# Kernel tuning notes

Measured on AMD Instinct MI355X. Metric: run time of the kernel, lower is better.

The kernel has to match this reference:

```python
import jax, jax.numpy as jnp
import numpy as np

N, E = 50000, 800000
DN, DE, H, C = 64, 64, 4, 2
DH = DN // H


def setup_inputs() -> dict:
    key = jax.random.key(0)
    ks = jax.random.split(key, 12)
    def lin(k, fan_in, fan_out):
        return jax.random.normal(k, (fan_in, fan_out), dtype=jnp.float32) / np.sqrt(fan_in)
    return {
        "node_features": jax.random.normal(ks[0], (N, DN), dtype=jnp.float32),
        "edge_features": jax.random.normal(ks[1], (E, DE), dtype=jnp.float32),
        "edge_index": jax.random.randint(ks[2], (2, E), 0, N, dtype=jnp.int64),
        "Wq": lin(ks[3], DN, DN),
        "Wk": lin(ks[4], DN, DN),
        "Wv": lin(ks[5], DN, DN),
        "We": lin(ks[6], DE, DN),
        "Wo": lin(ks[7], DN, DN),
        "W1": lin(ks[8], 2 * DN + DE, DE),
        "b1": jnp.zeros((DE,), dtype=jnp.float32),
        "W2": lin(ks[9], DE, C),
        "b2": jnp.zeros((C,), dtype=jnp.float32),
    }


def reference(node_features, edge_features, edge_index, Wq, Wk, Wv, We, Wo, W1, b1, W2, b2):
    n = node_features.shape[0]
    src, tgt = edge_index[0], edge_index[1]

    # --- NodeAttention: multi-head attention over incoming edges ---
    q = (node_features @ Wq).reshape(n, H, DH)
    k = (node_features @ Wk).reshape(n, H, DH)
    v = (node_features @ Wv).reshape(n, H, DH)
    ep = (edge_features @ We).reshape(-1, H, DH)          # [E,H,DH]

    scores = jnp.sum(q[tgt] * (k[src] + ep), axis=-1) / np.sqrt(DH)  # [E,H]
    smax = jax.ops.segment_max(scores, tgt, num_segments=n)          # [N,H]
    ex = jnp.exp(scores - smax[tgt])
    denom = jax.ops.segment_sum(ex, tgt, num_segments=n)
    alpha = ex / (denom[tgt] + 1e-9)                                 # [E,H]

    msg = (alpha[..., None] * (v[src] + ep)).reshape(-1, H * DH)     # [E,DN]
    agg = jax.ops.segment_sum(msg, tgt, num_segments=n)              # [N,DN]
    new_nodes = node_features + agg @ Wo                             # residual

    # --- edge classifier: gather endpoints, concat edge feats, MLP+GELU ---
    edge_repr = jnp.concatenate([new_nodes[src], new_nodes[tgt], edge_features], axis=-1)
    h = jax.nn.gelu(edge_repr @ W1 + b1, approximate=False)
    return h @ W2 + b2
```

## Files before the change

kernel.cpp:

```cpp
#include <hip/hip_runtime.h>
#include <math.h>

typedef __attribute__((ext_vector_type(8))) short bf16x8;
typedef __attribute__((ext_vector_type(4))) float f32x4;

__device__ __forceinline__ short f2bf(float f) {
    unsigned u = __float_as_uint(f);
    unsigned r = (u + 0x7FFFu + ((u >> 16) & 1u)) >> 16;
    return (short)r;
}
__device__ __forceinline__ float bf2f(short s) {
    return __uint_as_float(((unsigned)(unsigned short)s) << 16);
}

__device__ __forceinline__ int swz(int row, int kbyte) {
    return kbyte ^ ((row & 7) << 4);
}

__global__ __launch_bounds__(256) void hist_kernel(
    const int* __restrict__ eidx, int* __restrict__ cnt, int E)
{
    for (long e = (long)blockIdx.x * blockDim.x + threadIdx.x; e < E;
         e += (long)gridDim.x * blockDim.x)
        atomicAdd(&cnt[eidx[E + e]], 1);
}

__global__ __launch_bounds__(256) void scanA_kernel(
    const int* __restrict__ cnt, int* __restrict__ tmp, int* __restrict__ bsum, int N)
{
    __shared__ int sa[256], sb_[256];
    int t = threadIdx.x;
    int i = blockIdx.x * 256 + t;
    int val = (i < N) ? cnt[i] : 0;
    sa[t] = val;
    __syncthreads();
    int* src = sa; int* dst = sb_;
    for (int off = 1; off < 256; off <<= 1) {
        int v2 = src[t];
        if (t >= off) v2 += src[t - off];
        dst[t] = v2;
        __syncthreads();
        int* tm = src; src = dst; dst = tm;
    }
    if (i < N) tmp[i] = src[t];
    if (t == 255) bsum[blockIdx.x] = src[255];
}

__global__ __launch_bounds__(256) void scanB_kernel(
    const int* __restrict__ bsum, int* __restrict__ boff, int NB)
{
    __shared__ int sa[256], sb_[256];
    int t = threadIdx.x;
    int val = (t < NB) ? bsum[t] : 0;
    sa[t] = val;
    __syncthreads();
    int* src = sa; int* dst = sb_;
    for (int off = 1; off < 256; off <<= 1) {
        int v2 = src[t];
        if (t >= off) v2 += src[t - off];
        dst[t] = v2;
        __syncthreads();
        int* tm = src; src = dst; dst = tm;
    }
    if (t < NB) boff[t] = src[t] - val;
}

__global__ __launch_bounds__(256) void scanC_kernel(
    const int* __restrict__ cnt, const int* __restrict__ tmp,
    const int* __restrict__ boff, int* __restrict__ cursor, int N)
{
    int i = blockIdx.x * 256 + threadIdx.x;
    if (i < N) cursor[i] = tmp[i] - cnt[i] + boff[blockIdx.x];
}

__global__ __launch_bounds__(256) void scatter_kernel(
    const int* __restrict__ eidx, int* __restrict__ cursor,
    int4* __restrict__ sortedq, int E)
{
    for (long e = (long)blockIdx.x * blockDim.x + threadIdx.x; e < E;
         e += (long)gridDim.x * blockDim.x) {
        int sr = eidx[e];
        int tg = eidx[E + e];
        int pos = atomicAdd(&cursor[tg], 1);
        sortedq[pos] = make_int4((int)e, sr, tg, 0);
    }
}

__global__ __launch_bounds__(256) void qkv_kernel(
    const float* __restrict__ x,
    const float* __restrict__ Wq, const float* __restrict__ Wk, const float* __restrict__ Wv,
    short* __restrict__ qb, short* __restrict__ kb_, short* __restrict__ vb, int N)
{
    __shared__ short sWT[12288];
    int t = threadIdx.x;
    for (int i = t; i < 4096; i += 256) {
        int k = i >> 6, n = i & 63;
        int kby = k * 2;
        int off = n * 128 + (swz(n, kby & ~15) | (kby & 15));
        *(short*)((char*)sWT + off) = f2bf(Wq[i]);
        *(short*)((char*)sWT + 8192 + off) = f2bf(Wk[i]);
        *(short*)((char*)sWT + 16384 + off) = f2bf(Wv[i]);
    }
    __syncthreads();

    int lane = t & 63, w = t >> 6;
    int tile = blockIdx.x;
    f32x4 acc[12];
    #pragma unroll
    for (int nt = 0; nt < 12; nt++) acc[nt] = (f32x4){0.f, 0.f, 0.f, 0.f};

    int gr = tile * 64 + w * 16 + (lane & 15);
    int grc = min(gr, N - 1);
    #pragma unroll
    for (int kk = 0; kk < 2; kk++) {
        const float* base = x + (size_t)grc * 64 + kk * 32 + (lane >> 4) * 8;
        float4 x0 = *(const float4*)(base);
        float4 x1 = *(const float4*)(base + 4);
        bf16x8 a;
        a[0] = f2bf(x0.x); a[1] = f2bf(x0.y); a[2] = f2bf(x0.z); a[3] = f2bf(x0.w);
        a[4] = f2bf(x1.x); a[5] = f2bf(x1.y); a[6] = f2bf(x1.z); a[7] = f2bf(x1.w);
        #pragma unroll
        for (int nt = 0; nt < 12; nt++) {
            int ng = nt * 16 + (lane & 15);
            int kby = kk * 64 + (lane >> 4) * 16;
            bf16x8 b = *(const bf16x8*)((const char*)sWT + ng * 128 + swz(ng, kby));
            acc[nt] = __builtin_amdgcn_mfma_f32_16x16x32_bf16(a, b, acc[nt], 0, 0, 0);
        }
    }
    #pragma unroll
    for (int nt = 0; nt < 12; nt++)
        #pragma unroll
        for (int r = 0; r < 4; r++) {
            int row = tile * 64 + w * 16 + (lane >> 4) * 4 + r;
            if (row < N) {
                int col = nt * 16 + (lane & 15);
                short vv = f2bf(acc[nt][r]);
                if (col < 64)       qb[(size_t)row * 64 + col] = vv;
                else if (col < 128) kb_[(size_t)row * 64 + col - 64] = vv;
                else                vb[(size_t)row * 64 + col - 128] = vv;
            }
        }
}

__device__ __forceinline__ void stage_w64T(const float* __restrict__ W, short* sWT, int t) {
    for (int i = t; i < 4096; i += 256) {
        int k = i >> 6, n = i & 63;
        short vv = f2bf(W[i]);
        int kby = k * 2;
        int off = n * 128 + (swz(n, kby & ~15) | (kby & 15));
        *(short*)((char*)sWT + off) = vv;
    }
}

__global__ __launch_bounds__(256) void edge_kernel(
    const float* __restrict__ ef, const int4* __restrict__ sortedq,
    const short* __restrict__ qb, const short* __restrict__ kb_,
    const short* __restrict__ vb, const float* __restrict__ We,
    float* __restrict__ denom, float* __restrict__ agg, int E)
{
    __shared__ short sWeT[4096];
    __shared__ float ep_lds[64 * 66];
    __shared__ float ex_lds[64 * 4];
    __shared__ int sedge[64], sidx[64], tidx[64];
    int t = threadIdx.x;
    stage_w64T(We, sWeT, t);
    __syncthreads();

    int lane = t & 63, w = t >> 6;
    int ntiles = E >> 6;
    for (int tile = blockIdx.x; tile < ntiles; tile += gridDim.x) {
        size_t tile64 = (size_t)tile * 64;
        if (t < 64) {
            int4 rec = sortedq[tile64 + t];
            sedge[t] = rec.x;
            sidx[t] = rec.y;
            tidx[t] = rec.z;
        }
        __syncthreads();

        {
            f32x4 acc[4];
            #pragma unroll
            for (int nt = 0; nt < 4; nt++) acc[nt] = (f32x4){0.f, 0.f, 0.f, 0.f};
            int erow = sedge[w * 16 + (lane & 15)];
            #pragma unroll
            for (int kk = 0; kk < 2; kk++) {
                const f32x4* base = (const f32x4*)(ef + (size_t)erow * 64 + kk * 32 + (lane >> 4) * 8);
                f32x4 x0 = __builtin_nontemporal_load(base);
                f32x4 x1 = __builtin_nontemporal_load(base + 1);
                bf16x8 a;
                a[0] = f2bf(x0.x); a[1] = f2bf(x0.y); a[2] = f2bf(x0.z); a[3] = f2bf(x0.w);
                a[4] = f2bf(x1.x); a[5] = f2bf(x1.y); a[6] = f2bf(x1.z); a[7] = f2bf(x1.w);
                #pragma unroll
                for (int nt = 0; nt < 4; nt++) {
                    int n = nt * 16 + (lane & 15);
                    int kby = kk * 64 + (lane >> 4) * 16;
                    bf16x8 b = *(const bf16x8*)((const char*)sWeT + n * 128 + swz(n, kby));
                    acc[nt] = __builtin_amdgcn_mfma_f32_16x16x32_bf16(a, b, acc[nt], 0, 0, 0);
                }
            }
            #pragma unroll
            for (int nt = 0; nt < 4; nt++)
                #pragma unroll
                for (int r = 0; r < 4; r++) {
                    int row = w * 16 + (lane >> 4) * 4 + r;
                    int col = nt * 16 + (lane & 15);
                    ep_lds[row * 66 + col] = acc[nt][r];
                }
        }
        __syncthreads();

        {
            int e_loc = t >> 2, h = t & 3;
            int src = sidx[e_loc], tgt = tidx[e_loc];
            const bf16x8* qp = (const bf16x8*)(qb + (size_t)tgt * 64 + h * 16);
            const bf16x8* kp = (const bf16x8*)(kb_ + (size_t)src * 64 + h * 16);
            bf16x8 q0 = qp[0], q1 = qp[1];
            bf16x8 k0 = kp[0], k1 = kp[1];
            const float* epp = ep_lds + e_loc * 66 + h * 16;
            float s = 0.f;
            #pragma unroll
            for (int j = 0; j < 8; j++) s += bf2f(q0[j]) * (bf2f(k0[j]) + epp[j]);
            #pragma unroll
            for (int j = 0; j < 8; j++) s += bf2f(q1[j]) * (bf2f(k1[j]) + epp[8 + j]);
            ex_lds[e_loc * 4 + h] = __expf(s * 0.25f);
        }
        __syncthreads();

        {
            int h = lane >> 4;
            float vv[16];
            #pragma unroll
            for (int i = 0; i < 16; i++)
                vv[i] = bf2f(vb[(size_t)sidx[w * 16 + i] * 64 + lane]);
            int cur = tidx[w * 16];
            float acc = 0.f, den = 0.f;
            #pragma unroll
            for (int i = 0; i < 16; i++) {
                int e_loc = w * 16 + i;
                int tg = tidx[e_loc];
                if (tg != cur) {
                    atomicAdd(&agg[(size_t)cur * 64 + lane], acc);
                    if ((lane & 15) == 0) atomicAdd(&denom[(size_t)cur * 4 + h], den);
                    acc = 0.f; den = 0.f; cur = tg;
                }
                float ex = ex_lds[e_loc * 4 + h];
                acc += ex * (vv[i] + ep_lds[e_loc * 66 + lane]);
                den += ex;
            }
            atomicAdd(&agg[(size_t)cur * 64 + lane], acc);
            if ((lane & 15) == 0) atomicAdd(&denom[(size_t)cur * 4 + h], den);
        }
        __syncthreads();
    }
}

__global__ __launch_bounds__(256) void wo_kernel(
    const float* __restrict__ agg, const float* __restrict__ denom,
    const float* __restrict__ x,
    const float* __restrict__ Wo, short* __restrict__ nnb, int N)
{
    __shared__ short sWT[4096];
    int t = threadIdx.x;
    stage_w64T(Wo, sWT, t);
    __syncthreads();

    int lane = t & 63, w = t >> 6;
    int tile = blockIdx.x;
    f32x4 acc[4];
    #pragma unroll
    for (int nt = 0; nt < 4; nt++) acc[nt] = (f32x4){0.f, 0.f, 0.f, 0.f};

    int gr = tile * 64 + w * 16 + (lane & 15);
    int grc = min(gr, N - 1);
    #pragma unroll
    for (int kk = 0; kk < 2; kk++) {
        int fbase = kk * 32 + (lane >> 4) * 8;
        int h = fbase >> 4;
        float d = denom[(size_t)grc * 4 + h] + 1e-9f;
        const float* base = agg + (size_t)grc * 64 + fbase;
        float4 x0 = *(const float4*)(base);
        float4 x1 = *(const float4*)(base + 4);
        float inv = 1.f / d;
        bf16x8 a;
        a[0] = f2bf(x0.x * inv); a[1] = f2bf(x0.y * inv);
        a[2] = f2bf(x0.z * inv); a[3] = f2bf(x0.w * inv);
        a[4] = f2bf(x1.x * inv); a[5] = f2bf(x1.y * inv);
        a[6] = f2bf(x1.z * inv); a[7] = f2bf(x1.w * inv);
        #pragma unroll
        for (int nt = 0; nt < 4; nt++) {
            int n = nt * 16 + (lane & 15);
            int kby = kk * 64 + (lane >> 4) * 16;
            bf16x8 b = *(const bf16x8*)((const char*)sWT + n * 128 + swz(n, kby));
            acc[nt] = __builtin_amdgcn_mfma_f32_16x16x32_bf16(a, b, acc[nt], 0, 0, 0);
        }
    }
    #pragma unroll
    for (int nt = 0; nt < 4; nt++)
        #pragma unroll
        for (int r = 0; r < 4; r++) {
            int row = tile * 64 + w * 16 + (lane >> 4) * 4 + r;
            if (row < N) {
                int col = nt * 16 + (lane & 15);
                nnb[(size_t)row * 64 + col] = f2bf(x[(size_t)row * 64 + col] + acc[nt][r]);
            }
        }
}

__global__ __launch_bounds__(256, 4) void cls_kernel(
    const short* __restrict__ nnb, const float* __restrict__ ef,
    const int* __restrict__ eidx,
    const float* __restrict__ W1, const float* __restrict__ b1,
    const float* __restrict__ W2, const float* __restrict__ b2,
    float* __restrict__ out, int E)
{
    __shared__ short sWt1[64 * 192];
    __shared__ float sW2[128];
    __shared__ float sb1[64];
    __shared__ float sb2[2];
    __shared__ int sidx[64], tidx[64];
    int t = threadIdx.x;
    for (int i = t; i < 192 * 64; i += 256) {
        int k = i >> 6, n = i & 63;
        short vv = f2bf(W1[i]);
        int kby = k * 2;
        int off = n * 384 + (swz(n, kby & ~15) | (kby & 15));
        *(short*)((char*)sWt1 + off) = vv;
    }
    if (t < 128) sW2[t] = W2[t];
    if (t < 64) sb1[t] = b1[t];
    if (t < 2) sb2[t] = b2[t];
    __syncthreads();

    int lane = t & 63, w = t >> 6;
    int ntiles = E >> 6;
    for (int tile = blockIdx.x; tile < ntiles; tile += gridDim.x) {
        size_t tile64 = (size_t)tile * 64;
        if (t < 64) {
            sidx[t] = eidx[tile64 + t];
            tidx[t] = eidx[(size_t)E + tile64 + t];
        }
        __syncthreads();

        f32x4 acc[4];
        #pragma unroll
        for (int nt = 0; nt < 4; nt++) acc[nt] = (f32x4){0.f, 0.f, 0.f, 0.f};

        int e16 = w * 16 + (lane & 15);
        #pragma unroll
        for (int kk = 0; kk < 6; kk++) {
            bf16x8 a;
            if (kk < 4) {
                int nd = (kk < 2) ? sidx[e16] : tidx[e16];
                a = *(const bf16x8*)(nnb + (size_t)nd * 64 + (kk & 1) * 32 + (lane >> 4) * 8);
            } else {
                const f32x4* p = (const f32x4*)(ef + (tile64 + (size_t)e16) * 64
                                                + (kk - 4) * 32 + (lane >> 4) * 8);
                f32x4 x0 = __builtin_nontemporal_load(p);
                f32x4 x1 = __builtin_nontemporal_load(p + 1);
                a[0] = f2bf(x0.x); a[1] = f2bf(x0.y); a[2] = f2bf(x0.z); a[3] = f2bf(x0.w);
                a[4] = f2bf(x1.x); a[5] = f2bf(x1.y); a[6] = f2bf(x1.z); a[7] = f2bf(x1.w);
            }
            #pragma unroll
            for (int nt = 0; nt < 4; nt++) {
                int n = nt * 16 + (lane & 15);
                int kby = kk * 64 + (lane >> 4) * 16;
                bf16x8 b = *(const bf16x8*)((const char*)sWt1 + n * 384 + swz(n, kby));
                acc[nt] = __builtin_amdgcn_mfma_f32_16x16x32_bf16(a, b, acc[nt], 0, 0, 0);
            }
        }

        #pragma unroll
        for (int r = 0; r < 4; r++) {
            float p0 = 0.f, p1 = 0.f;
            #pragma unroll
            for (int nt = 0; nt < 4; nt++) {
                int col = nt * 16 + (lane & 15);
                float h = acc[nt][r] + sb1[col];
                float g = 0.5f * h * (1.f + erff(h * 0.70710678118654752f));
                p0 += g * sW2[col * 2 + 0];
                p1 += g * sW2[col * 2 + 1];
            }
            #pragma unroll
            for (int o = 1; o < 16; o <<= 1) {
                p0 += __shfl_xor(p0, o, 64);
                p1 += __shfl_xor(p1, o, 64);
            }
            if ((lane & 15) == 0) {
                int row = w * 16 + (lane >> 4) * 4 + r;
                out[(tile64 + (size_t)row) * 2 + 0] = p0 + sb2[0];
                out[(tile64 + (size_t)row) * 2 + 1] = p1 + sb2[1];
            }
        }
        __syncthreads();
    }
}

extern "C" void kernel_launch(void* const* d_in, const int* in_sizes, int n_in,
                              void* d_out, int out_size, void* d_ws, size_t ws_size,
                              hipStream_t stream)
{
    const float* node = (const float*)d_in[0];
    const float* ef   = (const float*)d_in[1];
    const int*   eidx = (const int*)d_in[2];
    const float* Wq   = (const float*)d_in[3];
    const float* Wk   = (const float*)d_in[4];
    const float* Wv   = (const float*)d_in[5];
    const float* We   = (const float*)d_in[6];
    const float* Wo   = (const float*)d_in[7];
    const float* W1   = (const float*)d_in[8];
    const float* b1   = (const float*)d_in[9];
    const float* W2   = (const float*)d_in[10];
    const float* b2   = (const float*)d_in[11];
    float* out = (float*)d_out;

    int N = in_sizes[0] / 64;
    int E = in_sizes[1] / 64;
    size_t N64 = (size_t)N * 64;
    int NB = (N + 255) / 256;

    int4*  sortedq = (int4*)d_ws;
    short* qb   = (short*)(sortedq + E);
    short* kb_  = qb + N64;
    short* vb   = kb_ + N64;
    short* nnb  = vb + N64;
    float* agg  = (float*)(nnb + N64);
    float* denom = agg + N64;
    int*   cnt   = (int*)(denom + (size_t)N * 4);
    int*   cursor = cnt + N;
    int*   tmp    = cursor + N;
    int*   bsum   = tmp + N;
    int*   boff   = bsum + 256;

    hipMemsetAsync(agg, 0, (N64 + (size_t)N * 4 + (size_t)N) * 4, stream);

    hist_kernel<<<2048, 256, 0, stream>>>(eidx, cnt, E);
    scanA_kernel<<<NB, 256, 0, stream>>>(cnt, tmp, bsum, N);
    scanB_kernel<<<1, 256, 0, stream>>>(bsum, boff, NB);
    scanC_kernel<<<NB, 256, 0, stream>>>(cnt, tmp, boff, cursor, N);
    scatter_kernel<<<2048, 256, 0, stream>>>(eidx, cursor, sortedq, E);
    qkv_kernel<<<(N + 63) / 64, 256, 0, stream>>>(node, Wq, Wk, Wv, qb, kb_, vb, N);
    edge_kernel<<<2048, 256, 0, stream>>>(ef, sortedq, qb, kb_, vb, We, denom, agg, E);
    wo_kernel<<<(N + 63) / 64, 256, 0, stream>>>(agg, denom, node, Wo, nnb, N);
    cls_kernel<<<2048, 256, 0, stream>>>(nnb, ef, eidx, W1, b1, W2, b2, out, E);
}
```

Before: 560.2 us.

## Make edge and classifier tiles wave-private, replacing block barriers with shuffles

In the edge kernel, each wave now owns a 16-edge slice. It loads the sorted index records into registers and shares them with shuffles, keeps its edge projection in a per-wave LDS slab, and passes exp scores by shuffle instead of through shared memory. This removes all per-tile __syncthreads. In the classifier kernel, every lane loads its own src/tgt indices directly rather than staging them in LDS behind barriers. The trade-off is per-iteration V gathers inside the accumulation loop instead of preloading all 16, and redundant index loads across lanes.

```diff
diff --git a/kernel.cpp b/kernel.cpp
--- a/kernel.cpp
+++ b/kernel.cpp
@@ -159,9 +159,7 @@
     float* __restrict__ denom, float* __restrict__ agg, int E)
 {
     __shared__ short sWeT[4096];
-    __shared__ float ep_lds[64 * 66];
-    __shared__ float ex_lds[64 * 4];
-    __shared__ int sedge[64], sidx[64], tidx[64];
+    __shared__ float ep_s[4][16][68];
     int t = threadIdx.x;
     stage_w64T(We, sWeT, t);
     __syncthreads();
@@ -169,25 +167,21 @@
     int lane = t & 63, w = t >> 6;
     int ntiles = E >> 6;
     for (int tile = blockIdx.x; tile < ntiles; tile += gridDim.x) {
-        size_t tile64 = (size_t)tile * 64;
-        if (t < 64) {
-            int4 rec = sortedq[tile64 + t];
-            sedge[t] = rec.x;
-            sidx[t] = rec.y;
-            tidx[t] = rec.z;
-        }
-        __syncthreads();
+        size_t base = (size_t)tile * 64 + w * 16;
+
+        int4 rec = make_int4(0, 0, 0, 0);
+        if (lane < 16) rec = sortedq[base + lane];
 
         {
+            int erow = __shfl(rec.x, lane & 15);
             f32x4 acc[4];
             #pragma unroll
             for (int nt = 0; nt < 4; nt++) acc[nt] = (f32x4){0.f, 0.f, 0.f, 0.f};
-            int erow = sedge[w * 16 + (lane & 15)];
             #pragma unroll
             for (int kk = 0; kk < 2; kk++) {
-                const f32x4* base = (const f32x4*)(ef + (size_t)erow * 64 + kk * 32 + (lane >> 4) * 8);
-                f32x4 x0 = __builtin_nontemporal_load(base);
-                f32x4 x1 = __builtin_nontemporal_load(base + 1);
+                const f32x4* bp = (const f32x4*)(ef + (size_t)erow * 64 + kk * 32 + (lane >> 4) * 8);
+                f32x4 x0 = __builtin_nontemporal_load(bp);
+                f32x4 x1 = __builtin_nontemporal_load(bp + 1);
                 bf16x8 a;
                 a[0] = f2bf(x0.x); a[1] = f2bf(x0.y); a[2] = f2bf(x0.z); a[3] = f2bf(x0.w);
                 a[4] = f2bf(x1.x); a[5] = f2bf(x1.y); a[6] = f2bf(x1.z); a[7] = f2bf(x1.w);
@@ -202,56 +196,54 @@
             #pragma unroll
             for (int nt = 0; nt < 4; nt++)
                 #pragma unroll
-                for (int r = 0; r < 4; r++) {
-                    int row = w * 16 + (lane >> 4) * 4 + r;
-                    int col = nt * 16 + (lane & 15);
-                    ep_lds[row * 66 + col] = acc[nt][r];
-                }
-        }
-        __syncthreads();
-
+                for (int r = 0; r < 4; r++)
+                    ep_s[w][(lane >> 4) * 4 + r][nt * 16 + (lane & 15)] = acc[nt][r];
+        }
+
+        float ex;
         {
-            int e_loc = t >> 2, h = t & 3;
-            int src = sidx[e_loc], tgt = tidx[e_loc];
-            const bf16x8* qp = (const bf16x8*)(qb + (size_t)tgt * 64 + h * 16);
-            const bf16x8* kp = (const bf16x8*)(kb_ + (size_t)src * 64 + h * 16);
+            int e_loc = lane >> 2, h = lane & 3;
+            int srcB = __shfl(rec.y, e_loc);
+            int tgtB = __shfl(rec.z, e_loc);
+            const bf16x8* qp = (const bf16x8*)(qb + (size_t)tgtB * 64 + h * 16);
+            const bf16x8* kp = (const bf16x8*)(kb_ + (size_t)srcB * 64 + h * 16);
             bf16x8 q0 = qp[0], q1 = qp[1];
             bf16x8 k0 = kp[0], k1 = kp[1];
-            const float* epp = ep_lds + e_loc * 66 + h * 16;
+            const f32x4* eprow = (const f32x4*)&ep_s[w][e_loc][h * 16];
+            f32x4 e0 = eprow[0], e1 = eprow[1], e2 = eprow[2], e3 = eprow[3];
             float s = 0.f;
             #pragma unroll
-            for (int j = 0; j < 8; j++) s += bf2f(q0[j]) * (bf2f(k0[j]) + epp[j]);
-            #pragma unroll
-            for (int j = 0; j < 8; j++) s += bf2f(q1[j]) * (bf2f(k1[j]) + epp[8 + j]);
-            ex_lds[e_loc * 4 + h] = __expf(s * 0.25f);
-        }
-        __syncthreads();
+            for (int j = 0; j < 4; j++) s += bf2f(q0[j]) * (bf2f(k0[j]) + e0[j]);
+            #pragma unroll
+            for (int j = 0; j < 4; j++) s += bf2f(q0[4 + j]) * (bf2f(k0[4 + j]) + e1[j]);
+            #pragma unroll
+            for (int j = 0; j < 4; j++) s += bf2f(q1[j]) * (bf2f(k1[j]) + e2[j]);
+            #pragma unroll
+            for (int j = 0; j < 4; j++) s += bf2f(q1[4 + j]) * (bf2f(k1[4 + j]) + e3[j]);
+            ex = __expf(s * 0.25f);
+        }
 
         {
             int h = lane >> 4;
-            float vv[16];
-            #pragma unroll
-            for (int i = 0; i < 16; i++)
-                vv[i] = bf2f(vb[(size_t)sidx[w * 16 + i] * 64 + lane]);
-            int cur = tidx[w * 16];
+            int cur = __shfl(rec.z, 0);
             float acc = 0.f, den = 0.f;
             #pragma unroll
             for (int i = 0; i < 16; i++) {
-                int e_loc = w * 16 + i;
-                int tg = tidx[e_loc];
+                int tg = __shfl(rec.z, i);
+                int si = __shfl(rec.y, i);
                 if (tg != cur) {
                     atomicAdd(&agg[(size_t)cur * 64 + lane], acc);
                     if ((lane & 15) == 0) atomicAdd(&denom[(size_t)cur * 4 + h], den);
                     acc = 0.f; den = 0.f; cur = tg;
                 }
-                float ex = ex_lds[e_loc * 4 + h];
-                acc += ex * (vv[i] + ep_lds[e_loc * 66 + lane]);
-                den += ex;
+                float exi = __shfl(ex, i * 4 + h);
+                float vvv = bf2f(vb[(size_t)si * 64 + lane]);
+                acc += exi * (vvv + ep_s[w][i][lane]);
+                den += exi;
             }
             atomicAdd(&agg[(size_t)cur * 64 + lane], acc);
             if ((lane & 15) == 0) atomicAdd(&denom[(size_t)cur * 4 + h], den);
         }
-        __syncthreads();
     }
 }
 
@@ -318,7 +310,6 @@
     __shared__ float sW2[128];
     __shared__ float sb1[64];
     __shared__ float sb2[2];
-    __shared__ int sidx[64], tidx[64];
     int t = threadIdx.x;
     for (int i = t; i < 192 * 64; i += 256) {
         int k = i >> 6, n = i & 63;
@@ -336,25 +327,22 @@
     int ntiles = E >> 6;
     for (int tile = blockIdx.x; tile < ntiles; tile += gridDim.x) {
         size_t tile64 = (size_t)tile * 64;
-        if (t < 64) {
-            sidx[t] = eidx[tile64 + t];
-            tidx[t] = eidx[(size_t)E + tile64 + t];
-        }
-        __syncthreads();
+        size_t e16 = tile64 + w * 16 + (lane & 15);
+        int srcn = eidx[e16];
+        int tgtn = eidx[(size_t)E + e16];
 
         f32x4 acc[4];
         #pragma unroll
         for (int nt = 0; nt < 4; nt++) acc[nt] = (f32x4){0.f, 0.f, 0.f, 0.f};
 
-        int e16 = w * 16 + (lane & 15);
         #pragma unroll
         for (int kk = 0; kk < 6; kk++) {
             bf16x8 a;
             if (kk < 4) {
-                int nd = (kk < 2) ? sidx[e16] : tidx[e16];
+                int nd = (kk < 2) ? srcn : tgtn;
                 a = *(const bf16x8*)(nnb + (size_t)nd * 64 + (kk & 1) * 32 + (lane >> 4) * 8);
             } else {
-                const f32x4* p = (const f32x4*)(ef + (tile64 + (size_t)e16) * 64
+                const f32x4* p = (const f32x4*)(ef + e16 * 64
                                                 + (kk - 4) * 32 + (lane >> 4) * 8);
                 f32x4 x0 = __builtin_nontemporal_load(p);
                 f32x4 x1 = __builtin_nontemporal_load(p + 1);
@@ -392,7 +380,6 @@
                 out[(tile64 + (size_t)row) * 2 + 1] = p1 + sb2[1];
             }
         }
-        __syncthreads();
     }
 }
 
```

Measured after the change: 700.8 us. +25.1%, slower.
